# Kernel tuning notes

Measured on AMD Instinct MI355X. Metric: run time of the kernel, lower is better.

The kernel has to match this reference:

```python
import jax, jax.numpy as jnp
import numpy as np

NEG_SLOPE = 0.2  # PyG GATConv default leaky_relu slope


def _gat_conv(x, src, dst, W, a_src, a_dst, b, num_nodes):
    # Linear transform: [N, F_out]
    h = x @ W
    # Per-node attention halves (heads=1): [N]
    alpha_s = h @ a_src
    alpha_d = h @ a_dst
    # Per-edge raw score for edge j->i: a_src.h_j + a_dst.h_i
    e = jax.nn.leaky_relu(alpha_s[src] + alpha_d[dst], NEG_SLOPE)
    # Softmax over edges grouped by destination node (numerically stable)
    m = jax.ops.segment_max(e, dst, num_segments=num_nodes)
    ex = jnp.exp(e - m[dst])
    denom = jax.ops.segment_sum(ex, dst, num_segments=num_nodes)
    coef = ex / denom[dst]
    # Attention-weighted aggregation of source features into destinations
    out = jax.ops.segment_sum(h[src] * coef[:, None], dst, num_segments=num_nodes)
    return out + b


def setup_inputs() -> dict:
    key = jax.random.key(0)
    ks = jax.random.split(key, 12)
    N, F_in, F_hid, F_out, E = 100000, 128, 64, 40, 1600000
    x = jax.random.normal(ks[0], (N, F_in), dtype=jnp.float32)
    edge_index = jax.random.randint(ks[1], (2, E), 0, N, dtype=jnp.int64)
    g = lambda k, shape, fan: jax.random.normal(k, shape, dtype=jnp.float32) * (1.0 / np.sqrt(fan))
    return {
        "x": x,
        "edge_index": edge_index,
        "W1": g(ks[2], (F_in, F_hid), F_in),
        "a_src1": g(ks[3], (F_hid,), F_hid),
        "a_dst1": g(ks[4], (F_hid,), F_hid),
        "b1": jnp.zeros((F_hid,), dtype=jnp.float32),
        "W2": g(ks[5], (F_hid, F_out), F_hid),
        "a_src2": g(ks[6], (F_out,), F_out),
        "a_dst2": g(ks[7], (F_out,), F_out),
        "b2": jnp.zeros((F_out,), dtype=jnp.float32),
    }


def reference(x, edge_index, W1, a_src1, a_dst1, b1, W2, a_src2, a_dst2, b2):
    N = x.shape[0]
    # PyG GATConv adds self loops by default
    loops = jnp.arange(N, dtype=edge_index.dtype)
    src = jnp.concatenate([edge_index[0], loops])
    dst = jnp.concatenate([edge_index[1], loops])
    h = _gat_conv(x, src, dst, W1, a_src1, a_dst1, b1, N)
    h = jax.nn.relu(h)
    # dropout p=0.5 is inactive in eval mode
    h = _gat_conv(h, src, dst, W2, a_src2, a_dst2, b2, N)
    return jax.nn.log_softmax(h, axis=-1)
```

## Files before the change

### kernel.cpp

```cpp
#include <hip/hip_runtime.h>
#include <math.h>


constexpr int F_IN = 128;
constexpr int F_H  = 64;
constexpr int F_O  = 40;
constexpr int NBMAX = 512;
constexpr int CHUNK = 8192;

using h2 = decltype(__builtin_amdgcn_cvt_pkrtz(0.f, 0.f));
typedef __attribute__((ext_vector_type(4))) float f32x4;
typedef __attribute__((ext_vector_type(8))) short s16x8;

__device__ __forceinline__ h2 u2h(unsigned u) { return __builtin_bit_cast(h2, u); }

__device__ __forceinline__ float fdot2f(h2 a, h2 b, float c) {
#if __has_builtin(__builtin_amdgcn_fdot2)
    return __builtin_amdgcn_fdot2(a, b, c, false);
#else
    return c + (float)a.x * (float)b.x + (float)a.y * (float)b.y;
#endif
}
__device__ __forceinline__ h2 pklo(unsigned a, unsigned b) {
    return u2h(__builtin_amdgcn_perm(a, b, 0x05040100u));
}
__device__ __forceinline__ h2 pkhi(unsigned a, unsigned b) {
    return u2h(__builtin_amdgcn_perm(a, b, 0x07060302u));
}
__device__ __forceinline__ unsigned short f2h(float f) {
    _Float16 x = (_Float16)f;
    return __builtin_bit_cast(unsigned short, x);
}
__device__ __forceinline__ void nt_store4(uint4* p, uint4 v) {
    __builtin_nontemporal_store(v.x, &p->x);
    __builtin_nontemporal_store(v.y, &p->y);
    __builtin_nontemporal_store(v.z, &p->z);
    __builtin_nontemporal_store(v.w, &p->w);
}
__device__ __forceinline__ void nt_storef4(float4* p, float4 v) {
    __builtin_nontemporal_store(v.x, &p->x);
    __builtin_nontemporal_store(v.y, &p->y);
    __builtin_nontemporal_store(v.z, &p->z);
    __builtin_nontemporal_store(v.w, &p->w);
}


__global__ __launch_bounds__(256) void k_binA(const int* __restrict__ dsts,
                                              int* __restrict__ bcnt,
                                              int E, int Et, int NB) {
    __shared__ int hist[NBMAX];
    for (int i = threadIdx.x; i < NB; i += 256) hist[i] = 0;
    __syncthreads();
    int e0 = blockIdx.x * 2048;
#pragma unroll
    for (int it = 0; it < 8; ++it) {
        int e = e0 + it * 256 + threadIdx.x;
        if (e < Et) {
            int d = (e < E) ? dsts[e] : (e - E);
            atomicAdd(&hist[d >> 8], 1);
        }
    }
    __syncthreads();
    for (int i = threadIdx.x; i < NB; i += 256) {
        int c = hist[i];
        if (c) atomicAdd(&bcnt[i], c);
    }
}

__global__ __launch_bounds__(NBMAX) void k_binB(const int* __restrict__ bcnt,
                                                int* __restrict__ bbase,
                                                int* __restrict__ bcur,
                                                int* __restrict__ rp,
                                                int NB, int N, int Et) {
    __shared__ int sc[NBMAX];
    int t = threadIdx.x;
    int v = (t < NB) ? bcnt[t] : 0;
    sc[t] = v; __syncthreads();
    int x = v;
    for (int o = 1; o < NBMAX; o <<= 1) {
        int y = (t >= o) ? sc[t - o] : 0;
        __syncthreads();
        x += y;
        sc[t] = x;
        __syncthreads();
    }
    if (t < NB) { int b = x - v; bbase[t] = b; bcur[t] = b; }
    if (t == 0) rp[N] = Et;
}

__global__ __launch_bounds__(256) void k_binC(const int* __restrict__ srcs,
                                              const int* __restrict__ dsts,
                                              int* __restrict__ bcur,
                                              unsigned* __restrict__ binned,
                                              int E, int Et, int NB) {
    __shared__ int hist[NBMAX];
    __shared__ int gbase[NBMAX];
    __shared__ int lcnt[NBMAX];
    int t = threadIdx.x;
    for (int i = t; i < NB; i += 256) hist[i] = 0;
    __syncthreads();
    int e0 = blockIdx.x * CHUNK;
#pragma unroll 4
    for (int it = 0; it < CHUNK / 256; ++it) {
        int e = e0 + it * 256 + t;
        if (e < Et) {
            int d = (e < E) ? dsts[e] : (e - E);
            atomicAdd(&hist[d >> 8], 1);
        }
    }
    __syncthreads();
    for (int i = t; i < NB; i += 256) {
        int c = hist[i];
        gbase[i] = c ? atomicAdd(&bcur[i], c) : 0;
        lcnt[i] = 0;
    }
    __syncthreads();
#pragma unroll 4
    for (int it = 0; it < CHUNK / 256; ++it) {
        int e = e0 + it * 256 + t;
        if (e < Et) {
            int s, d;
            if (e < E) { s = srcs[e]; d = dsts[e]; } else { s = e - E; d = s; }
            int b = d >> 8;
            int p = atomicAdd(&lcnt[b], 1);
            binned[gbase[b] + p] = (unsigned)s | ((unsigned)(d & 255) << 24);
        }
    }
}

__global__ __launch_bounds__(256) void k_binD(const unsigned* __restrict__ binned,
                                              const int* __restrict__ bbase,
                                              const int* __restrict__ bcur,
                                              int* __restrict__ rp,
                                              int* __restrict__ csr, int N) {
    __shared__ int hist[256];
    __shared__ int sc[256];
    __shared__ int lcnt[256];
    int b = blockIdx.x, t = threadIdx.x;
    int base = bbase[b], end = bcur[b];
    hist[t] = 0; __syncthreads();
    for (int j = base + t; j < end; j += 256)
        atomicAdd(&hist[binned[j] >> 24], 1);
    __syncthreads();
    int v = hist[t];
    sc[t] = v; __syncthreads();
    int x = v;
    for (int o = 1; o < 256; o <<= 1) {
        int y = (t >= o) ? sc[t - o] : 0;
        __syncthreads();
        x += y;
        sc[t] = x;
        __syncthreads();
    }
    int pref = x - v;
    int g = (b << 8) + t;
    if (g < N) rp[g] = base + pref;
    sc[t] = pref;
    lcnt[t] = 0;
    __syncthreads();
    for (int j = base + t; j < end; j += 256) {
        unsigned w = binned[j];
        int v2 = (int)(w >> 24);
        int s = (int)(w & 0xFFFFFFu);
        int p = atomicAdd(&lcnt[v2], 1);
        csr[base + sc[v2] + p] = s;
    }
}


__global__ __launch_bounds__(256) void k_wsplit(const float* __restrict__ W,
                                                unsigned short* __restrict__ WhiT,
                                                unsigned short* __restrict__ WloT) {
    int i = blockIdx.x * 256 + threadIdx.x;
    if (i >= F_IN * F_H) return;
    int k = i >> 6, c = i & 63;
    float w = W[i];
    unsigned u = __float_as_uint(w);
    unsigned hi = u & 0xFFFF0000u;
    float d = w - __uint_as_float(hi);
    WhiT[c * F_IN + k] = (unsigned short)(hi >> 16);
    WloT[c * F_IN + k] = (unsigned short)(__float_as_uint(d) >> 16);
}


__global__ __launch_bounds__(256) void k_gemm1m(const float* __restrict__ x,
                                                const unsigned short* __restrict__ WhiT,
                                                const unsigned short* __restrict__ WloT,
                                                const float* __restrict__ avs,
                                                const float* __restrict__ avd,
                                                unsigned short* __restrict__ h,
                                                float* __restrict__ as,
                                                float* __restrict__ ad, int N) {
    __shared__ __align__(16) float xs[64][132];
    unsigned short (*hs)[72] = (unsigned short(*)[72])xs;
    const int t = threadIdx.x;
    const int wv = t >> 6;
    const int lane = t & 63;
    const int lrow = lane & 15;
    const int lk8 = lane >> 4;
    const int r0 = blockIdx.x * 64;

    {
        const float4* xg = (const float4*)x;
#pragma unroll
        for (int it = 0; it < 8; ++it) {
            int flat = it * 256 + t;
            int row = flat >> 5, c4 = flat & 31;
            int grow = min(r0 + row, N - 1);
            float4 v = xg[(size_t)grow * 32 + c4];
            *(float4*)&xs[row][c4 * 4] = v;
        }
    }
    __syncthreads();

    s16x8 ah[4], al[4];
#pragma unroll
    for (int kt = 0; kt < 4; ++kt) {
        const float* rp_ = &xs[wv * 16 + lrow][kt * 32 + lk8 * 8];
        float4 a = *(const float4*)rp_;
        float4 b = *(const float4*)(rp_ + 4);
        float e0[8] = {a.x, a.y, a.z, a.w, b.x, b.y, b.z, b.w};
        unsigned uh[4], ul[4];
#pragma unroll
        for (int p = 0; p < 4; ++p) {
            float a0 = e0[2 * p], a1 = e0[2 * p + 1];
            unsigned u0 = __float_as_uint(a0), u1 = __float_as_uint(a1);
            float d0 = a0 - __uint_as_float(u0 & 0xFFFF0000u);
            float d1 = a1 - __uint_as_float(u1 & 0xFFFF0000u);
            uh[p] = __builtin_amdgcn_perm(u1, u0, 0x07060302u);
            ul[p] = __builtin_amdgcn_perm(__float_as_uint(d1), __float_as_uint(d0), 0x07060302u);
        }
        ah[kt] = __builtin_bit_cast(s16x8, make_uint4(uh[0], uh[1], uh[2], uh[3]));
        al[kt] = __builtin_bit_cast(s16x8, make_uint4(ul[0], ul[1], ul[2], ul[3]));
    }
    __syncthreads();

    f32x4 acc[4] = {};
#pragma unroll
    for (int kt = 0; kt < 4; ++kt) {
#pragma unroll
        for (int ct = 0; ct < 4; ++ct) {
            const int boff = (ct * 16 + lrow) * F_IN + kt * 32 + lk8 * 8;
            s16x8 bh = *(const s16x8*)&WhiT[boff];
            s16x8 bl = *(const s16x8*)&WloT[boff];
            acc[ct] = __builtin_amdgcn_mfma_f32_16x16x32_bf16(ah[kt], bh, acc[ct], 0, 0, 0);
            acc[ct] = __builtin_amdgcn_mfma_f32_16x16x32_bf16(al[kt], bh, acc[ct], 0, 0, 0);
            acc[ct] = __builtin_amdgcn_mfma_f32_16x16x32_bf16(ah[kt], bl, acc[ct], 0, 0, 0);
        }
    }

    float avs_c[4], avd_c[4];
#pragma unroll
    for (int ct = 0; ct < 4; ++ct) {
        avs_c[ct] = avs[ct * 16 + lrow];
        avd_c[ct] = avd[ct * 16 + lrow];
    }
#pragma unroll
    for (int r = 0; r < 4; ++r) {
        float ps = acc[0][r] * avs_c[0] + acc[1][r] * avs_c[1]
                 + acc[2][r] * avs_c[2] + acc[3][r] * avs_c[3];
        float pd = acc[0][r] * avd_c[0] + acc[1][r] * avd_c[1]
                 + acc[2][r] * avd_c[2] + acc[3][r] * avd_c[3];
#pragma unroll
        for (int o = 8; o; o >>= 1) {
            ps += __shfl_xor(ps, o, 16);
            pd += __shfl_xor(pd, o, 16);
        }
        int orow = r0 + wv * 16 + lk8 * 4 + r;
        if (lrow == 0 && orow < N) { as[orow] = ps; ad[orow] = pd; }
    }

#pragma unroll
    for (int ct = 0; ct < 4; ++ct)
#pragma unroll
        for (int r = 0; r < 4; ++r)
            hs[wv * 16 + lk8 * 4 + r][ct * 16 + lrow] = f2h(acc[ct][r]);
    __syncthreads();
    const int row = t >> 2, ch = t & 3;
    const int grow = r0 + row;
    if (grow < N) {
        uint4 v0 = *(const uint4*)&hs[row][ch * 16];
        uint4 v1 = *(const uint4*)&hs[row][ch * 16 + 8];
        uint4* gp = (uint4*)(h + (size_t)grow * F_H + ch * 16);
        nt_store4(gp, v0);
        nt_store4(gp + 1, v1);
    }
}


__global__ __launch_bounds__(256) void k_gemm2(const unsigned short* __restrict__ xin,
                                               const float* __restrict__ W,
                                               const float* __restrict__ avs,
                                               const float* __restrict__ avd,
                                               unsigned short* __restrict__ h,
                                               float* __restrict__ as,
                                               float* __restrict__ ad, int N) {
    __shared__ __align__(16) float Ws[F_H * F_O];
    for (int i = threadIdx.x; i < F_H * F_O; i += 256) Ws[i] = W[i];
    __syncthreads();
    int t = threadIdx.x;
    int r0 = blockIdx.x * 64 + (t >> 3) * 2;
    int l = t & 7;
    if (r0 >= N) return;
    const uint2* xa = (const uint2*)(xin + (size_t)r0 * F_H);
    const uint2* xb = (const uint2*)(xin + (size_t)(r0 + 1) * F_H);
    float acca[5] = {}, accb[5] = {};
#pragma unroll
    for (int k4 = 0; k4 < F_H / 4; ++k4) {
        uint2 ua = xa[k4];
        uint2 ub = xb[k4];
        h2 a01 = u2h(ua.x), a23 = u2h(ua.y);
        h2 b01 = u2h(ub.x), b23 = u2h(ub.y);
        float xva[4] = {(float)a01.x, (float)a01.y, (float)a23.x, (float)a23.y};
        float xvb[4] = {(float)b01.x, (float)b01.y, (float)b23.x, (float)b23.y};
        int kb = k4 * 4;
#pragma unroll
        for (int kk = 0; kk < 4; ++kk) {
            const float* wr = &Ws[(kb + kk) * F_O + l];
            float w0 = wr[0], w1 = wr[8], w2 = wr[16], w3 = wr[24], w4 = wr[32];
            float xs = xva[kk];
            acca[0] += xs * w0; acca[1] += xs * w1; acca[2] += xs * w2;
            acca[3] += xs * w3; acca[4] += xs * w4;
            float ys = xvb[kk];
            accb[0] += ys * w0; accb[1] += ys * w1; accb[2] += ys * w2;
            accb[3] += ys * w3; accb[4] += ys * w4;
        }
    }
    float psa = 0.f, pda = 0.f, psb = 0.f, pdb = 0.f;
    unsigned short* ra = h + (size_t)r0 * F_H;
    unsigned short* rb = h + (size_t)(r0 + 1) * F_H;
#pragma unroll
    for (int cc = 0; cc < 5; ++cc) {
        int c = l + 8 * cc;
        ra[c] = f2h(acca[cc]);
        rb[c] = f2h(accb[cc]);
        float vs = avs[c], vd = avd[c];
        psa += acca[cc] * vs; pda += acca[cc] * vd;
        psb += accb[cc] * vs; pdb += accb[cc] * vd;
    }
#pragma unroll
    for (int pp = 0; pp < 3; ++pp) {
        int c = 40 + l * 3 + pp;
        ra[c] = 0; rb[c] = 0;
    }
#pragma unroll
    for (int o = 4; o; o >>= 1) {
        psa += __shfl_xor(psa, o, 8);
        pda += __shfl_xor(pda, o, 8);
        psb += __shfl_xor(psb, o, 8);
        pdb += __shfl_xor(pdb, o, 8);
    }
    if (l == 0) { as[r0] = psa; ad[r0] = pda; as[r0 + 1] = psb; ad[r0 + 1] = pdb; }
}


template <int FOUT, bool RELU, bool LOGSM, bool F16OUT>
__global__ __launch_bounds__(256) void k_agg(const int* __restrict__ rp,
                                             const int* __restrict__ csr,
                                             const float* __restrict__ as,
                                             const float* __restrict__ ad,
                                             const uint4* __restrict__ h4,
                                             const float* __restrict__ bias,
                                             void* __restrict__ outv, int N) {
    constexpr int CAP = 64;
    __shared__ __align__(16) uint2 wsb[4][8][CAP + 2];
    const int w = threadIdx.x >> 6;
    const int g = (threadIdx.x >> 3) & 7;
    const int c = threadIdx.x & 7;
    const int i = blockIdx.x * 32 + (threadIdx.x >> 3);
    if (i >= N) return;
    const int start = rp[i], end = rp[i + 1];
    const int deg = end - start;
    const int dm = min(deg, CAP);
    const int dmR8 = (dm + 7) & ~7;
    const float adi = ad[i];

    for (int idx = c; idx < dm; idx += 8) {
        int srcn = __builtin_nontemporal_load(&csr[start + idx]);
        float e = as[srcn] + adi;
        e = fmaxf(e, 0.2f * e);
        wsb[w][g][idx] = make_uint2(__float_as_uint(__expf(e)), (unsigned)srcn);
    }
    {
        int idx = dm + c;
        if (idx < dmR8) wsb[w][g][idx] = make_uint2(0u, (unsigned)i);
    }

    const uint4* pw = (const uint4*)wsb[w][g];
    float acc[8] = {}, acc2[8] = {};
    float sacc = 0.f;
    const int noct = dmR8 >> 3;
    for (int q = 0; q < noct; ++q) {
        uint4 m0 = pw[4 * q];
        uint4 m1 = pw[4 * q + 1];
        uint4 m2 = pw[4 * q + 2];
        uint4 m3 = pw[4 * q + 3];
        uint4 hv0 = h4[((size_t)m0.y << 3) + c];
        uint4 hv1 = h4[((size_t)m0.w << 3) + c];
        uint4 hv2 = h4[((size_t)m1.y << 3) + c];
        uint4 hv3 = h4[((size_t)m1.w << 3) + c];
        uint4 hv4 = h4[((size_t)m2.y << 3) + c];
        uint4 hv5 = h4[((size_t)m2.w << 3) + c];
        uint4 hv6 = h4[((size_t)m3.y << 3) + c];
        uint4 hv7 = h4[((size_t)m3.w << 3) + c];
        float w0 = __uint_as_float(m0.x), w1 = __uint_as_float(m0.z);
        float w2 = __uint_as_float(m1.x), w3 = __uint_as_float(m1.z);
        float w4 = __uint_as_float(m2.x), w5 = __uint_as_float(m2.z);
        float w6 = __uint_as_float(m3.x), w7 = __uint_as_float(m3.z);
        sacc += ((w0 + w1) + (w2 + w3)) + ((w4 + w5) + (w6 + w7));
        h2 wp0 = __builtin_amdgcn_cvt_pkrtz(w0, w1);
        h2 wp1 = __builtin_amdgcn_cvt_pkrtz(w2, w3);
        h2 wp2 = __builtin_amdgcn_cvt_pkrtz(w4, w5);
        h2 wp3 = __builtin_amdgcn_cvt_pkrtz(w6, w7);
        acc[0] = fdot2f(wp0, pklo(hv1.x, hv0.x), acc[0]);
        acc[1] = fdot2f(wp0, pkhi(hv1.x, hv0.x), acc[1]);
        acc[2] = fdot2f(wp0, pklo(hv1.y, hv0.y), acc[2]);
        acc[3] = fdot2f(wp0, pkhi(hv1.y, hv0.y), acc[3]);
        acc[4] = fdot2f(wp0, pklo(hv1.z, hv0.z), acc[4]);
        acc[5] = fdot2f(wp0, pkhi(hv1.z, hv0.z), acc[5]);
        acc[6] = fdot2f(wp0, pklo(hv1.w, hv0.w), acc[6]);
        acc[7] = fdot2f(wp0, pkhi(hv1.w, hv0.w), acc[7]);
        acc2[0] = fdot2f(wp1, pklo(hv3.x, hv2.x), acc2[0]);
        acc2[1] = fdot2f(wp1, pkhi(hv3.x, hv2.x), acc2[1]);
        acc2[2] = fdot2f(wp1, pklo(hv3.y, hv2.y), acc2[2]);
        acc2[3] = fdot2f(wp1, pkhi(hv3.y, hv2.y), acc2[3]);
        acc2[4] = fdot2f(wp1, pklo(hv3.z, hv2.z), acc2[4]);
        acc2[5] = fdot2f(wp1, pkhi(hv3.z, hv2.z), acc2[5]);
        acc2[6] = fdot2f(wp1, pklo(hv3.w, hv2.w), acc2[6]);
        acc2[7] = fdot2f(wp1, pkhi(hv3.w, hv2.w), acc2[7]);
        acc[0] = fdot2f(wp2, pklo(hv5.x, hv4.x), acc[0]);
        acc[1] = fdot2f(wp2, pkhi(hv5.x, hv4.x), acc[1]);
        acc[2] = fdot2f(wp2, pklo(hv5.y, hv4.y), acc[2]);
        acc[3] = fdot2f(wp2, pkhi(hv5.y, hv4.y), acc[3]);
        acc[4] = fdot2f(wp2, pklo(hv5.z, hv4.z), acc[4]);
        acc[5] = fdot2f(wp2, pkhi(hv5.z, hv4.z), acc[5]);
        acc[6] = fdot2f(wp2, pklo(hv5.w, hv4.w), acc[6]);
        acc[7] = fdot2f(wp2, pkhi(hv5.w, hv4.w), acc[7]);
        acc2[0] = fdot2f(wp3, pklo(hv7.x, hv6.x), acc2[0]);
        acc2[1] = fdot2f(wp3, pkhi(hv7.x, hv6.x), acc2[1]);
        acc2[2] = fdot2f(wp3, pklo(hv7.y, hv6.y), acc2[2]);
        acc2[3] = fdot2f(wp3, pkhi(hv7.y, hv6.y), acc2[3]);
        acc2[4] = fdot2f(wp3, pklo(hv7.z, hv6.z), acc2[4]);
        acc2[5] = fdot2f(wp3, pkhi(hv7.z, hv6.z), acc2[5]);
        acc2[6] = fdot2f(wp3, pklo(hv7.w, hv6.w), acc2[6]);
        acc2[7] = fdot2f(wp3, pkhi(hv7.w, hv6.w), acc2[7]);
    }

    for (int j = start + dm; j < end; ++j) {
        int srcn = __builtin_nontemporal_load(&csr[j]);
        float e = as[srcn] + adi;
        e = fmaxf(e, 0.2f * e);
        float wv = __expf(e);
        sacc += wv;
        uint4 hv = h4[((size_t)srcn << 3) + c];
        h2 wp = __builtin_amdgcn_cvt_pkrtz(wv, 0.f);
        acc[0] = fdot2f(wp, pklo(hv.x, hv.x), acc[0]);
        acc[1] = fdot2f(wp, pkhi(hv.x, hv.x), acc[1]);
        acc[2] = fdot2f(wp, pklo(hv.y, hv.y), acc[2]);
        acc[3] = fdot2f(wp, pkhi(hv.y, hv.y), acc[3]);
        acc[4] = fdot2f(wp, pklo(hv.z, hv.z), acc[4]);
        acc[5] = fdot2f(wp, pkhi(hv.z, hv.z), acc[5]);
        acc[6] = fdot2f(wp, pklo(hv.w, hv.w), acc[6]);
        acc[7] = fdot2f(wp, pkhi(hv.w, hv.w), acc[7]);
    }

#pragma unroll
    for (int k = 0; k < 8; ++k) acc[k] += acc2[k];
    float inv = 1.f / sacc;

    if (!LOGSM) {
        float r[8];
#pragma unroll
        for (int k = 0; k < 8; ++k) {
            r[k] = fmaf(acc[k], inv, bias[8 * c + k]);
            if (RELU) r[k] = fmaxf(r[k], 0.f);
        }
        if (F16OUT) {
            unsigned short* oh = (unsigned short*)outv;
            unsigned u0 = (unsigned)f2h(r[0]) | ((unsigned)f2h(r[1]) << 16);
            unsigned u1 = (unsigned)f2h(r[2]) | ((unsigned)f2h(r[3]) << 16);
            unsigned u2 = (unsigned)f2h(r[4]) | ((unsigned)f2h(r[5]) << 16);
            unsigned u3 = (unsigned)f2h(r[6]) | ((unsigned)f2h(r[7]) << 16);
            nt_store4((uint4*)(oh + (size_t)i * F_H + 8 * c),
                      make_uint4(u0, u1, u2, u3));
        } else {
            float* out = (float*)outv;
            float4* op = (float4*)(out + (size_t)i * FOUT + 8 * c);
            nt_storef4(op, make_float4(r[0], r[1], r[2], r[3]));
            nt_storef4(op + 1, make_float4(r[4], r[5], r[6], r[7]));
        }
    } else {
        float* out = (float*)outv;
        constexpr int VC = FOUT / 8;
        bool act = (c < VC);
        float v[8];
#pragma unroll
        for (int k = 0; k < 8; ++k) {
            float bv = bias[act ? 8 * c + k : 0];
            v[k] = act ? fmaf(acc[k], inv, bv) : -INFINITY;
        }
        float mx = v[0];
#pragma unroll
        for (int k = 1; k < 8; ++k) mx = fmaxf(mx, v[k]);
#pragma unroll
        for (int o = 1; o <= 4; o <<= 1) mx = fmaxf(mx, __shfl_xor(mx, o));
        float es = 0.f;
        if (act) {
#pragma unroll
            for (int k = 0; k < 8; ++k) es += __expf(v[k] - mx);
        }
#pragma unroll
        for (int o = 1; o <= 4; o <<= 1) es += __shfl_xor(es, o);
        if (act) {
            float lse = mx + __logf(es);
            float4* op = (float4*)(out + (size_t)i * FOUT + 8 * c);
            nt_storef4(op, make_float4(v[0] - lse, v[1] - lse, v[2] - lse, v[3] - lse));
            nt_storef4(op + 1, make_float4(v[4] - lse, v[5] - lse, v[6] - lse, v[7] - lse));
        }
    }
}


extern "C" void kernel_launch(void* const* d_in, const int* in_sizes, int n_in,
                              void* d_out, int out_size, void* d_ws, size_t ws_size,
                              hipStream_t stream) {
    const float* x   = (const float*)d_in[0];
    const int* edges = (const int*)d_in[1];
    const float* W1  = (const float*)d_in[2];
    const float* av_s1 = (const float*)d_in[3];
    const float* av_d1 = (const float*)d_in[4];
    const float* b1  = (const float*)d_in[5];
    const float* W2  = (const float*)d_in[6];
    const float* av_s2 = (const float*)d_in[7];
    const float* av_d2 = (const float*)d_in[8];
    const float* b2  = (const float*)d_in[9];
    float* out = (float*)d_out;

    const int N  = in_sizes[0] / F_IN;
    const int E  = in_sizes[1] / 2;
    const int Et = E + N;
    const int NB = (N + 255) >> 8;

    char* p = (char*)d_ws;
    auto alloc = [&](size_t bytes) {
        char* q = p;
        p += (bytes + 255) & ~(size_t)255;
        return (void*)q;
    };
    unsigned short* h1 = (unsigned short*)alloc((size_t)N * F_H * 2);
    unsigned short* out1h = (unsigned short*)alloc((size_t)N * F_H * 2);
    float* as1    = (float*)alloc((size_t)N * 4);
    float* ad1    = (float*)alloc((size_t)N * 4);
    float* as2    = (float*)alloc((size_t)N * 4);
    float* ad2    = (float*)alloc((size_t)N * 4);
    int* rp       = (int*)alloc((size_t)(N + 1) * 4);
    int* bcnt     = (int*)alloc(NBMAX * 4);
    int* bbase    = (int*)alloc(NBMAX * 4);
    int* bcur     = (int*)alloc(NBMAX * 4);
    unsigned* binned = (unsigned*)alloc((size_t)Et * 4);
    int* csr      = (int*)alloc((size_t)Et * 4);
    unsigned short* WhiT = (unsigned short*)alloc((size_t)F_H * F_IN * 2);
    unsigned short* WloT = (unsigned short*)alloc((size_t)F_H * F_IN * 2);
    (void)n_in; (void)out_size; (void)ws_size;

    const int* srcs = edges;
    const int* dsts = edges + E;

    hipMemsetAsync(bcnt, 0, NBMAX * 4, stream);

    k_wsplit<<<(F_IN * F_H + 255) / 256, 256, 0, stream>>>(W1, WhiT, WloT);
    k_binA<<<(Et + 2047) / 2048, 256, 0, stream>>>(dsts, bcnt, E, Et, NB);
    k_binB<<<1, NBMAX, 0, stream>>>(bcnt, bbase, bcur, rp, NB, N, Et);
    k_binC<<<(Et + CHUNK - 1) / CHUNK, 256, 0, stream>>>(srcs, dsts, bcur, binned, E, Et, NB);
    k_binD<<<NB, 256, 0, stream>>>(binned, bbase, bcur, rp, csr, N);

    k_gemm1m<<<(N + 63) / 64, 256, 0, stream>>>(x, WhiT, WloT, av_s1, av_d1, h1, as1, ad1, N);
    int gAgg = (N + 31) / 32;
    k_agg<F_H, true, false, true><<<gAgg, 256, 0, stream>>>(rp, csr, as1, ad1,
                                                            (const uint4*)h1, b1, out1h, N);
    k_gemm2<<<(N + 63) / 64, 256, 0, stream>>>(out1h, W2, av_s2, av_d2, h1, as2, ad2, N);
    k_agg<F_O, false, true, false><<<gAgg, 256, 0, stream>>>(rp, csr, as2, ad2,
                                                             (const uint4*)h1, b2, out, N);
}
```

Before: 293.7 us.

## Sort CSR neighbors by source range, prefetch W fragments, use cached h stores

```diff
diff --git a/kernel.cpp b/kernel.cpp
--- a/kernel.cpp
+++ b/kernel.cpp
@@ -7,6 +7,7 @@
 constexpr int F_O  = 40;
 constexpr int NBMAX = 512;
 constexpr int CHUNK = 8192;
+constexpr int NKEY  = 2048;
 
 using h2 = decltype(__builtin_amdgcn_cvt_pkrtz(0.f, 0.f));
 typedef __attribute__((ext_vector_type(4))) float f32x4;
@@ -30,12 +31,6 @@
 __device__ __forceinline__ unsigned short f2h(float f) {
     _Float16 x = (_Float16)f;
     return __builtin_bit_cast(unsigned short, x);
-}
-__device__ __forceinline__ void nt_store4(uint4* p, uint4 v) {
-    __builtin_nontemporal_store(v.x, &p->x);
-    __builtin_nontemporal_store(v.y, &p->y);
-    __builtin_nontemporal_store(v.z, &p->z);
-    __builtin_nontemporal_store(v.w, &p->w);
 }
 __device__ __forceinline__ void nt_storef4(float4* p, float4 v) {
     __builtin_nontemporal_store(v.x, &p->x);
@@ -128,42 +123,51 @@
     }
 }
 
+
 __global__ __launch_bounds__(256) void k_binD(const unsigned* __restrict__ binned,
                                               const int* __restrict__ bbase,
                                               const int* __restrict__ bcur,
                                               int* __restrict__ rp,
                                               int* __restrict__ csr, int N) {
-    __shared__ int hist[256];
-    __shared__ int sc[256];
-    __shared__ int lcnt[256];
+    __shared__ int hist[NKEY];
+    __shared__ int sc2[NKEY];
+    __shared__ int lcnt[NKEY];
+    __shared__ int tsum[256];
     int b = blockIdx.x, t = threadIdx.x;
     int base = bbase[b], end = bcur[b];
-    hist[t] = 0; __syncthreads();
-    for (int j = base + t; j < end; j += 256)
-        atomicAdd(&hist[binned[j] >> 24], 1);
-    __syncthreads();
-    int v = hist[t];
-    sc[t] = v; __syncthreads();
-    int x = v;
+    for (int k = t; k < NKEY; k += 256) { hist[k] = 0; lcnt[k] = 0; }
+    __syncthreads();
+    for (int j = base + t; j < end; j += 256) {
+        unsigned w = binned[j];
+        int key = ((int)(w >> 24) << 3) | (int)((w & 0xFFFFFFu) >> 14);
+        atomicAdd(&hist[key], 1);
+    }
+    __syncthreads();
+    int myk = t << 3;
+    int s = 0;
+#pragma unroll
+    for (int k = 0; k < 8; ++k) s += hist[myk + k];
+    tsum[t] = s; __syncthreads();
+    int x = s;
     for (int o = 1; o < 256; o <<= 1) {
-        int y = (t >= o) ? sc[t - o] : 0;
+        int y = (t >= o) ? tsum[t - o] : 0;
         __syncthreads();
         x += y;
-        sc[t] = x;
+        tsum[t] = x;
         __syncthreads();
     }
-    int pref = x - v;
+    int run = x - s;
     int g = (b << 8) + t;
-    if (g < N) rp[g] = base + pref;
-    sc[t] = pref;
-    lcnt[t] = 0;
+    if (g < N) rp[g] = base + run;
+#pragma unroll
+    for (int k = 0; k < 8; ++k) { sc2[myk + k] = run; run += hist[myk + k]; }
     __syncthreads();
     for (int j = base + t; j < end; j += 256) {
         unsigned w = binned[j];
-        int v2 = (int)(w >> 24);
-        int s = (int)(w & 0xFFFFFFu);
-        int p = atomicAdd(&lcnt[v2], 1);
-        csr[base + sc[v2] + p] = s;
+        int src = (int)(w & 0xFFFFFFu);
+        int key = ((int)(w >> 24) << 3) | (src >> 14);
+        int p = atomicAdd(&lcnt[key], 1);
+        csr[base + sc2[key] + p] = src;
     }
 }
 
@@ -183,14 +187,14 @@
 }
 
 
-__global__ __launch_bounds__(256) void k_gemm1m(const float* __restrict__ x,
-                                                const unsigned short* __restrict__ WhiT,
-                                                const unsigned short* __restrict__ WloT,
-                                                const float* __restrict__ avs,
-                                                const float* __restrict__ avd,
-                                                unsigned short* __restrict__ h,
-                                                float* __restrict__ as,
-                                                float* __restrict__ ad, int N) {
+__global__ __launch_bounds__(256, 2) void k_gemm1m(const float* __restrict__ x,
+                                                   const unsigned short* __restrict__ WhiT,
+                                                   const unsigned short* __restrict__ WloT,
+                                                   const float* __restrict__ avs,
+                                                   const float* __restrict__ avd,
+                                                   unsigned short* __restrict__ h,
+                                                   float* __restrict__ as,
+                                                   float* __restrict__ ad, int N) {
     __shared__ __align__(16) float xs[64][132];
     unsigned short (*hs)[72] = (unsigned short(*)[72])xs;
     const int t = threadIdx.x;
@@ -211,6 +215,16 @@
             *(float4*)&xs[row][c4 * 4] = v;
         }
     }
+
+    s16x8 bh[4][4], bl[4][4];
+#pragma unroll
+    for (int kt = 0; kt < 4; ++kt)
+#pragma unroll
+        for (int ct = 0; ct < 4; ++ct) {
+            const int boff = (ct * 16 + lrow) * F_IN + kt * 32 + lk8 * 8;
+            bh[kt][ct] = *(const s16x8*)&WhiT[boff];
+            bl[kt][ct] = *(const s16x8*)&WloT[boff];
+        }
     __syncthreads();
 
     s16x8 ah[4], al[4];
@@ -240,12 +254,9 @@
     for (int kt = 0; kt < 4; ++kt) {
 #pragma unroll
         for (int ct = 0; ct < 4; ++ct) {
-            const int boff = (ct * 16 + lrow) * F_IN + kt * 32 + lk8 * 8;
-            s16x8 bh = *(const s16x8*)&WhiT[boff];
-            s16x8 bl = *(const s16x8*)&WloT[boff];
-            acc[ct] = __builtin_amdgcn_mfma_f32_16x16x32_bf16(ah[kt], bh, acc[ct], 0, 0, 0);
-            acc[ct] = __builtin_amdgcn_mfma_f32_16x16x32_bf16(al[kt], bh, acc[ct], 0, 0, 0);
-            acc[ct] = __builtin_amdgcn_mfma_f32_16x16x32_bf16(ah[kt], bl, acc[ct], 0, 0, 0);
+            acc[ct] = __builtin_amdgcn_mfma_f32_16x16x32_bf16(ah[kt], bh[kt][ct], acc[ct], 0, 0, 0);
+            acc[ct] = __builtin_amdgcn_mfma_f32_16x16x32_bf16(al[kt], bh[kt][ct], acc[ct], 0, 0, 0);
+            acc[ct] = __builtin_amdgcn_mfma_f32_16x16x32_bf16(ah[kt], bl[kt][ct], acc[ct], 0, 0, 0);
         }
     }
 
@@ -282,8 +293,7 @@
         uint4 v0 = *(const uint4*)&hs[row][ch * 16];
         uint4 v1 = *(const uint4*)&hs[row][ch * 16 + 8];
         uint4* gp = (uint4*)(h + (size_t)grow * F_H + ch * 16);
-        nt_store4(gp, v0);
-        nt_store4(gp + 1, v1);
+        gp[0] = v0; gp[1] = v1;
     }
 }
 
@@ -481,8 +491,7 @@
             unsigned u1 = (unsigned)f2h(r[2]) | ((unsigned)f2h(r[3]) << 16);
             unsigned u2 = (unsigned)f2h(r[4]) | ((unsigned)f2h(r[5]) << 16);
             unsigned u3 = (unsigned)f2h(r[6]) | ((unsigned)f2h(r[7]) << 16);
-            nt_store4((uint4*)(oh + (size_t)i * F_H + 8 * c),
-                      make_uint4(u0, u1, u2, u3));
+            *(uint4*)(oh + (size_t)i * F_H + 8 * c) = make_uint4(u0, u1, u2, u3);
         } else {
             float* out = (float*)outv;
             float4* op = (float4*)(out + (size_t)i * FOUT + 8 * c);
```

Measured after the change: 292.5 us. About the same (-0.4%).
